# Optimization experiments

Hardware: AMD Instinct MI355X
Metric: run time of the kernel (lower is better)

## Reference

```python
import jax, jax.numpy as jnp
import numpy as np

N = 50000
E = 800000
F_IN = 128
HID = 64
HEADS = 4
NEG_SLOPE = 0.2  # PyG GATConv default negative_slope


def segment_softmax(e, dst, num_segments):
    # numerically stable softmax over edges grouped by destination node
    m = jax.ops.segment_max(e, dst, num_segments=num_segments)
    ex = jnp.exp(e - m[dst])
    s = jax.ops.segment_sum(ex, dst, num_segments=num_segments)
    return ex / (s[dst] + 1e-16)


def gat_conv(x, src, dst, W, a_src, a_dst, bias, heads, out_ch, concat):
    n = x.shape[0]
    h = (x @ W).reshape(n, heads, out_ch)          # [N,H,C]
    alpha_s = (h * a_src).sum(-1)                  # [N,H]
    alpha_d = (h * a_dst).sum(-1)                  # [N,H]
    e = jax.nn.leaky_relu(alpha_s[src] + alpha_d[dst], NEG_SLOPE)  # [E,H]
    alpha = segment_softmax(e, dst, n)             # [E,H]
    out = jax.ops.segment_sum(h[src] * alpha[:, :, None], dst, num_segments=n)  # [N,H,C]
    out = out.reshape(n, heads * out_ch) if concat else out.mean(axis=1)
    return out + bias


def setup_inputs() -> dict:
    key = jax.random.key(0)
    ks = jax.random.split(key, 16)

    def lin(k, i, o):
        return (jax.random.normal(k, (i, o), jnp.float32) / np.float32(np.sqrt(i)))

    def att(k, h, c):
        return jax.random.normal(k, (h, c), jnp.float32) * np.float32(0.1)

    x = jax.random.normal(ks[0], (N, F_IN), jnp.float32)
    edge_index = jax.random.randint(ks[1], (2, E), 0, N, dtype=jnp.int32)
    return {
        "x": x,
        "W_emb": lin(ks[2], F_IN, HID), "b_emb": jnp.zeros(HID, jnp.float32),
        "W0": lin(ks[3], HID, HEADS * HID), "as0": att(ks[4], HEADS, HID), "ad0": att(ks[5], HEADS, HID), "b0": jnp.zeros(HEADS * HID, jnp.float32),
        "W1": lin(ks[6], HEADS * HID, HEADS * HID), "as1": att(ks[7], HEADS, HID), "ad1": att(ks[8], HEADS, HID), "b1": jnp.zeros(HEADS * HID, jnp.float32),
        "W2": lin(ks[9], HEADS * HID, HID), "as2": att(ks[10], 1, HID), "ad2": att(ks[11], 1, HID), "b2": jnp.zeros(HID, jnp.float32),
        "Wo1": lin(ks[12], HID, HID // 2), "bo1": jnp.zeros(HID // 2, jnp.float32),
        "Wo2": lin(ks[13], HID // 2, 1), "bo2": jnp.zeros(1, jnp.float32),
        "edge_index": edge_index,
    }


def reference(x, W_emb, b_emb, W0, as0, ad0, b0, W1, as1, ad1, b1, W2, as2, ad2, b2, Wo1, bo1, Wo2, bo2, edge_index):
    n = x.shape[0]
    loop = jnp.arange(n, dtype=edge_index.dtype)  # PyG GATConv adds self-loops
    src = jnp.concatenate([edge_index[0], loop])
    dst = jnp.concatenate([edge_index[1], loop])
    h = jax.nn.relu(x @ W_emb + b_emb)
    h = jax.nn.relu(gat_conv(h, src, dst, W0, as0, ad0, b0, HEADS, HID, True))   # dropout=identity (eval)
    h = jax.nn.relu(gat_conv(h, src, dst, W1, as1, ad1, b1, HEADS, HID, True))
    h = gat_conv(h, src, dst, W2, as2, ad2, b2, 1, HID, False)
    h = jax.nn.relu(h @ Wo1 + bo1)
    return h @ Wo2 + bo2  # [N,1]
```

## Files before the change

### kernel.cpp

```cpp
#include <hip/hip_runtime.h>

typedef _Float16 h8_t __attribute__((ext_vector_type(8)));
typedef _Float16 h4_t __attribute__((ext_vector_type(4)));
typedef float floatx4 __attribute__((ext_vector_type(4)));

__device__ __forceinline__ float leaky(float v) { return v >= 0.f ? v : 0.2f * v; }

__global__ void hist_kernel(const int* __restrict__ dst, int E, int* __restrict__ cnt) {
    int e = blockIdx.x * blockDim.x + threadIdx.x;
    if (e < E) atomicAdd(&cnt[dst[e]], 1);
}

__global__ __launch_bounds__(256) void blocksum_kernel(const int* __restrict__ cnt, int N,
                                                       int* __restrict__ bsum) {
    __shared__ int red[256];
    int tid = threadIdx.x;
    int idx = blockIdx.x * 256 + tid;
    red[tid] = idx < N ? cnt[idx] + 1 : 0;
    __syncthreads();
#pragma unroll
    for (int off = 128; off >= 1; off >>= 1) {
        if (tid < off) red[tid] += red[tid + off];
        __syncthreads();
    }
    if (tid == 0) bsum[blockIdx.x] = red[0];
}

__global__ __launch_bounds__(256) void scanbsum_kernel(int* __restrict__ bsum, int nb,
                                                       int* __restrict__ total) {
    __shared__ int part[256];
    int tid = threadIdx.x;
    int per = (nb + 255) / 256;
    int s0 = tid * per, s1 = min(s0 + per, nb);
    int s = 0;
    for (int i = s0; i < s1; i++) s += bsum[i];
    part[tid] = s;
    __syncthreads();
    for (int off = 1; off < 256; off <<= 1) {
        int v = (tid >= off) ? part[tid - off] : 0;
        __syncthreads();
        part[tid] += v;
        __syncthreads();
    }
    int base = (tid == 0) ? 0 : part[tid - 1];
    for (int i = s0; i < s1; i++) {
        int v = bsum[i];
        bsum[i] = base;
        base += v;
    }
    if (tid == 255) *total = part[255];
}

__global__ __launch_bounds__(256) void rowptr_kernel(const int* __restrict__ cnt,
                                                     const int* __restrict__ bsum, int N,
                                                     int* __restrict__ row_ptr,
                                                     int* __restrict__ cursor) {
    __shared__ int lds[256];
    int tid = threadIdx.x;
    int idx = blockIdx.x * 256 + tid;
    int v = idx < N ? cnt[idx] + 1 : 0;
    lds[tid] = v;
    __syncthreads();
    for (int off = 1; off < 256; off <<= 1) {
        int t = (tid >= off) ? lds[tid - off] : 0;
        __syncthreads();
        lds[tid] += t;
        __syncthreads();
    }
    if (idx < N) {
        int p = bsum[blockIdx.x] + lds[tid] - v;
        row_ptr[idx] = p;
        cursor[idx] = p;
    }
}

__global__ void scatter_kernel(const int* __restrict__ src, const int* __restrict__ dst,
                               int E, int N, int* __restrict__ cursor, int* __restrict__ csr_src) {
    int e = blockIdx.x * blockDim.x + threadIdx.x;
    if (e >= E + N) return;
    int s, d;
    if (e < E) { s = src[e]; d = dst[e]; }
    else       { s = e - E;  d = s; }
    int pos = atomicAdd(&cursor[d], 1);
    csr_src[pos] = s;
}

__global__ void prep_weight_kernel(const float* __restrict__ W,
                                   _Float16* __restrict__ Wh, _Float16* __restrict__ Wl,
                                   int K, int N) {
    int idx = blockIdx.x * blockDim.x + threadIdx.x;
    if (idx >= K * N) return;
    int k = idx / N, n = idx % N;
    float v = W[idx];
    _Float16 hi = (_Float16)v;
    _Float16 lo = (_Float16)(v - (float)hi);
    size_t o = ((size_t)(k >> 3) * N + n) * 8 + (k & 7);
    Wh[o] = hi; Wl[o] = lo;
}

__global__ void prep_act_kernel(const float* __restrict__ X,
                                _Float16* __restrict__ Ph, _Float16* __restrict__ Pl,
                                int M, int Mpad, int Kg, int K) {
    int idx = blockIdx.x * blockDim.x + threadIdx.x;
    if (idx >= Mpad * Kg) return;
    int row = idx / Kg, kg = idx - row * Kg;
    float vs[8] = {0.f, 0.f, 0.f, 0.f, 0.f, 0.f, 0.f, 0.f};
    if (row < M) {
        const float4* p = (const float4*)(X + (size_t)row * K + kg * 8);
        float4 a = p[0], b = p[1];
        vs[0] = a.x; vs[1] = a.y; vs[2] = a.z; vs[3] = a.w;
        vs[4] = b.x; vs[5] = b.y; vs[6] = b.z; vs[7] = b.w;
    }
    h8_t hh, hl;
#pragma unroll
    for (int j = 0; j < 8; j++) {
        _Float16 hi = (_Float16)vs[j];
        hh[j] = hi;
        hl[j] = (_Float16)(vs[j] - (float)hi);
    }
    size_t o = ((size_t)kg * Mpad + row) * 8;
    *reinterpret_cast<h8_t*>(Ph + o) = hh;
    *reinterpret_cast<h8_t*>(Pl + o) = hl;
}

__global__ __launch_bounds__(256) void gemm_emb_kernel(
        const _Float16* __restrict__ Ah, const _Float16* __restrict__ Al,
        const _Float16* __restrict__ Bh, const _Float16* __restrict__ Bl,
        const float* __restrict__ bias,
        _Float16* __restrict__ Ph, _Float16* __restrict__ Pl,
        int Mpad, int M, int K) {
    const int Nn = 64;
    __shared__ _Float16 stH[4][16][72];
    __shared__ _Float16 stL[4][16][72];
    int tid = threadIdx.x;
    int wv = tid >> 6, lane = tid & 63;
    int m16 = lane & 15, quad = lane >> 4;
    int row0 = blockIdx.x * 128 + wv * 32;

    floatx4 acc[2][4];
#pragma unroll
    for (int t = 0; t < 2; t++)
#pragma unroll
        for (int c = 0; c < 4; c++)
#pragma unroll
            for (int i = 0; i < 4; i++) acc[t][c][i] = 0.f;

    size_t aoff = ((size_t)quad * Mpad + row0 + m16) * 8;
    size_t boff = ((size_t)quad * Nn + m16) * 8;
    const size_t aStep = (size_t)Mpad * 32;
    const size_t bStep = (size_t)Nn * 32;

    for (int kt = 0; kt < K; kt += 32) {
        h8_t ah0 = *reinterpret_cast<const h8_t*>(Ah + aoff);
        h8_t ah1 = *reinterpret_cast<const h8_t*>(Ah + aoff + 128);
        h8_t al0 = *reinterpret_cast<const h8_t*>(Al + aoff);
        h8_t al1 = *reinterpret_cast<const h8_t*>(Al + aoff + 128);
#pragma unroll
        for (int c = 0; c < 4; c++) {
            h8_t bh = *reinterpret_cast<const h8_t*>(Bh + boff + c * 128);
            h8_t bl = *reinterpret_cast<const h8_t*>(Bl + boff + c * 128);
            acc[0][c] = __builtin_amdgcn_mfma_f32_16x16x32_f16(ah0, bh, acc[0][c], 0, 0, 0);
            acc[1][c] = __builtin_amdgcn_mfma_f32_16x16x32_f16(ah1, bh, acc[1][c], 0, 0, 0);
            acc[0][c] = __builtin_amdgcn_mfma_f32_16x16x32_f16(ah0, bl, acc[0][c], 0, 0, 0);
            acc[1][c] = __builtin_amdgcn_mfma_f32_16x16x32_f16(ah1, bl, acc[1][c], 0, 0, 0);
            acc[0][c] = __builtin_amdgcn_mfma_f32_16x16x32_f16(al0, bh, acc[0][c], 0, 0, 0);
            acc[1][c] = __builtin_amdgcn_mfma_f32_16x16x32_f16(al1, bh, acc[1][c], 0, 0, 0);
        }
        aoff += aStep; boff += bStep;
    }

#pragma unroll
    for (int t = 0; t < 2; t++) {
#pragma unroll
        for (int c = 0; c < 4; c++) {
            float bv = bias[c * 16 + m16];
#pragma unroll
            for (int i = 0; i < 4; i++) {
                float v = fmaxf(acc[t][c][i] + bv, 0.f);
                _Float16 hi = (_Float16)v;
                stH[wv][quad * 4 + i][c * 16 + m16] = hi;
                stL[wv][quad * 4 + i][c * 16 + m16] = (_Float16)(v - (float)hi);
            }
        }
        __syncthreads();
        int rowChunk = row0 + t * 16;
#pragma unroll
        for (int it = 0; it < 2; it++) {
            int lid = it * 64 + lane;
            int kg = lid >> 4, rloc = lid & 15;
            h8_t vh = *reinterpret_cast<const h8_t*>(&stH[wv][rloc][kg * 8]);
            h8_t vl = *reinterpret_cast<const h8_t*>(&stL[wv][rloc][kg * 8]);
            size_t o = ((size_t)kg * Mpad + rowChunk + rloc) * 8;
            *reinterpret_cast<h8_t*>(Ph + o) = vh;
            *reinterpret_cast<h8_t*>(Pl + o) = vl;
        }
        __syncthreads();
    }
}

__global__ __launch_bounds__(256) void gemm_gat_kernel(
        const _Float16* __restrict__ Ah, const _Float16* __restrict__ Al,
        const _Float16* __restrict__ Bh, const _Float16* __restrict__ Bl,
        const float* __restrict__ a_src, const float* __restrict__ a_dst,
        _Float16* __restrict__ hOut, float* __restrict__ aS, float* __restrict__ aD,
        int Mpad, int M, int K) {
    const int Nn = 256;
    __shared__ _Float16 st[4][16][136];
    int tid = threadIdx.x;
    int wv = tid >> 6, lane = tid & 63;
    int m16 = lane & 15, quad = lane >> 4;
    int row0 = blockIdx.x * 128 + wv * 32;
    int colBase = blockIdx.y * 128;

    floatx4 acc[2][8];
#pragma unroll
    for (int t = 0; t < 2; t++)
#pragma unroll
        for (int c = 0; c < 8; c++)
#pragma unroll
            for (int i = 0; i < 4; i++) acc[t][c][i] = 0.f;

    size_t aoff = ((size_t)quad * Mpad + row0 + m16) * 8;
    size_t boff = ((size_t)quad * Nn + colBase + m16) * 8;
    const size_t aStep = (size_t)Mpad * 32;
    const size_t bStep = (size_t)Nn * 32;

    for (int kt = 0; kt < K; kt += 32) {
        h8_t ah0 = *reinterpret_cast<const h8_t*>(Ah + aoff);
        h8_t ah1 = *reinterpret_cast<const h8_t*>(Ah + aoff + 128);
        h8_t al0 = *reinterpret_cast<const h8_t*>(Al + aoff);
        h8_t al1 = *reinterpret_cast<const h8_t*>(Al + aoff + 128);
#pragma unroll
        for (int c = 0; c < 8; c++) {
            h8_t bh = *reinterpret_cast<const h8_t*>(Bh + boff + c * 128);
            h8_t bl = *reinterpret_cast<const h8_t*>(Bl + boff + c * 128);
            acc[0][c] = __builtin_amdgcn_mfma_f32_16x16x32_f16(ah0, bh, acc[0][c], 0, 0, 0);
            acc[1][c] = __builtin_amdgcn_mfma_f32_16x16x32_f16(ah1, bh, acc[1][c], 0, 0, 0);
            acc[0][c] = __builtin_amdgcn_mfma_f32_16x16x32_f16(ah0, bl, acc[0][c], 0, 0, 0);
            acc[1][c] = __builtin_amdgcn_mfma_f32_16x16x32_f16(ah1, bl, acc[1][c], 0, 0, 0);
            acc[0][c] = __builtin_amdgcn_mfma_f32_16x16x32_f16(al0, bh, acc[0][c], 0, 0, 0);
            acc[1][c] = __builtin_amdgcn_mfma_f32_16x16x32_f16(al1, bh, acc[1][c], 0, 0, 0);
        }
        aoff += aStep; boff += bStep;
    }

    float asv[8], adv[8];
#pragma unroll
    for (int c = 0; c < 8; c++) {
        asv[c] = a_src[colBase + c * 16 + m16];
        adv[c] = a_dst[colBase + c * 16 + m16];
    }
    int hb = colBase >> 6;
#pragma unroll
    for (int t = 0; t < 2; t++) {
#pragma unroll
        for (int i = 0; i < 4; i++) {
            int r = row0 + t * 16 + quad * 4 + i;
            float s0 = 0.f, d0 = 0.f, s1 = 0.f, d1 = 0.f;
#pragma unroll
            for (int c = 0; c < 8; c++) {
                float v = acc[t][c][i];
                if (c < 4) { s0 += v * asv[c]; d0 += v * adv[c]; }
                else       { s1 += v * asv[c]; d1 += v * adv[c]; }
            }
#pragma unroll
            for (int off = 1; off < 16; off <<= 1) {
                s0 += __shfl_xor(s0, off);
                d0 += __shfl_xor(d0, off);
                s1 += __shfl_xor(s1, off);
                d1 += __shfl_xor(d1, off);
            }
            if (m16 == 0 && r < M) {
                aS[r * 4 + hb] = s0;     aD[r * 4 + hb] = d0;
                aS[r * 4 + hb + 1] = s1; aD[r * 4 + hb + 1] = d1;
            }
        }
    }

#pragma unroll
    for (int t = 0; t < 2; t++) {
#pragma unroll
        for (int c = 0; c < 8; c++)
#pragma unroll
            for (int i = 0; i < 4; i++)
                st[wv][quad * 4 + i][c * 16 + m16] = (_Float16)acc[t][c][i];
        __syncthreads();
        int rowChunk = row0 + t * 16;
#pragma unroll
        for (int it = 0; it < 4; it++) {
            int lid = it * 64 + lane;
            int rloc = lid >> 4, u = lid & 15;
            h8_t v = *reinterpret_cast<const h8_t*>(&st[wv][rloc][u * 8]);
            *reinterpret_cast<h8_t*>(hOut + (size_t)(rowChunk + rloc) * 256 + colBase + u * 8) = v;
        }
        __syncthreads();
    }
}

__global__ __launch_bounds__(256) void gemm_l2_kernel(
        const _Float16* __restrict__ Ah, const _Float16* __restrict__ Al,
        const _Float16* __restrict__ Bh, const _Float16* __restrict__ Bl,
        const float* __restrict__ a_src, const float* __restrict__ a_dst,
        _Float16* __restrict__ hOut, float* __restrict__ aS, float* __restrict__ aD,
        int Mpad, int M, int K) {
    const int Nn = 64;
    __shared__ _Float16 st[4][16][72];
    int tid = threadIdx.x;
    int wv = tid >> 6, lane = tid & 63;
    int m16 = lane & 15, quad = lane >> 4;
    int row0 = blockIdx.x * 128 + wv * 32;

    floatx4 acc[2][4];
#pragma unroll
    for (int t = 0; t < 2; t++)
#pragma unroll
        for (int c = 0; c < 4; c++)
#pragma unroll
            for (int i = 0; i < 4; i++) acc[t][c][i] = 0.f;

    size_t aoff = ((size_t)quad * Mpad + row0 + m16) * 8;
    size_t boff = ((size_t)quad * Nn + m16) * 8;
    const size_t aStep = (size_t)Mpad * 32;
    const size_t bStep = (size_t)Nn * 32;

    for (int kt = 0; kt < K; kt += 32) {
        h8_t ah0 = *reinterpret_cast<const h8_t*>(Ah + aoff);
        h8_t ah1 = *reinterpret_cast<const h8_t*>(Ah + aoff + 128);
        h8_t al0 = *reinterpret_cast<const h8_t*>(Al + aoff);
        h8_t al1 = *reinterpret_cast<const h8_t*>(Al + aoff + 128);
#pragma unroll
        for (int c = 0; c < 4; c++) {
            h8_t bh = *reinterpret_cast<const h8_t*>(Bh + boff + c * 128);
            h8_t bl = *reinterpret_cast<const h8_t*>(Bl + boff + c * 128);
            acc[0][c] = __builtin_amdgcn_mfma_f32_16x16x32_f16(ah0, bh, acc[0][c], 0, 0, 0);
            acc[1][c] = __builtin_amdgcn_mfma_f32_16x16x32_f16(ah1, bh, acc[1][c], 0, 0, 0);
            acc[0][c] = __builtin_amdgcn_mfma_f32_16x16x32_f16(ah0, bl, acc[0][c], 0, 0, 0);
            acc[1][c] = __builtin_amdgcn_mfma_f32_16x16x32_f16(ah1, bl, acc[1][c], 0, 0, 0);
            acc[0][c] = __builtin_amdgcn_mfma_f32_16x16x32_f16(al0, bh, acc[0][c], 0, 0, 0);
            acc[1][c] = __builtin_amdgcn_mfma_f32_16x16x32_f16(al1, bh, acc[1][c], 0, 0, 0);
        }
        aoff += aStep; boff += bStep;
    }

    float asv[4], adv[4];
#pragma unroll
    for (int c = 0; c < 4; c++) {
        asv[c] = a_src[c * 16 + m16];
        adv[c] = a_dst[c * 16 + m16];
    }
#pragma unroll
    for (int t = 0; t < 2; t++) {
#pragma unroll
        for (int i = 0; i < 4; i++) {
            int r = row0 + t * 16 + quad * 4 + i;
            float s0 = 0.f, d0 = 0.f;
#pragma unroll
            for (int c = 0; c < 4; c++) {
                float v = acc[t][c][i];
                s0 += v * asv[c]; d0 += v * adv[c];
            }
#pragma unroll
            for (int off = 1; off < 16; off <<= 1) {
                s0 += __shfl_xor(s0, off);
                d0 += __shfl_xor(d0, off);
            }
            if (m16 == 0 && r < M) { aS[r] = s0; aD[r] = d0; }
        }
    }

#pragma unroll
    for (int t = 0; t < 2; t++) {
#pragma unroll
        for (int c = 0; c < 4; c++)
#pragma unroll
            for (int i = 0; i < 4; i++)
                st[wv][quad * 4 + i][c * 16 + m16] = (_Float16)acc[t][c][i];
        __syncthreads();
        int rowChunk = row0 + t * 16;
#pragma unroll
        for (int it = 0; it < 2; it++) {
            int lid = it * 64 + lane;
            int rloc = lid >> 3, u = lid & 7;
            h8_t v = *reinterpret_cast<const h8_t*>(&st[wv][rloc][u * 8]);
            *reinterpret_cast<h8_t*>(hOut + (size_t)(rowChunk + rloc) * 64 + u * 8) = v;
        }
        __syncthreads();
    }
}

__global__ __launch_bounds__(256) void aggregate4_kernel(const _Float16* __restrict__ hsrc,
                                                         const float* __restrict__ alpha_s,
                                                         const float* __restrict__ alpha_d,
                                                         const int* __restrict__ row_ptr,
                                                         const int* __restrict__ csr_src,
                                                         const float* __restrict__ bias,
                                                         _Float16* __restrict__ outH,
                                                         _Float16* __restrict__ outL,
                                                         int N, int Mpad) {
    __shared__ float wlds[4][64][4];
    __shared__ int   slds[4][64];
    int wv = threadIdx.x >> 6, lane = threadIdx.x & 63;
    int node = blockIdx.x * 4 + wv;
    if (node >= N) return;
    int rs = row_ptr[node], re = row_ptr[node + 1];
    int head = lane >> 4, c4 = (lane & 15) * 4;
    float4 ad4 = *(const float4*)(alpha_d + (size_t)node * 4);

    float m0 = -1e30f, m1 = -1e30f, m2 = -1e30f, m3 = -1e30f;
    for (int base = rs; base < re; base += 64) {
        int i = base + lane;
        if (i < re) {
            int s = csr_src[i];
            float4 as = *(const float4*)(alpha_s + (size_t)s * 4);
            m0 = fmaxf(m0, leaky(as.x + ad4.x));
            m1 = fmaxf(m1, leaky(as.y + ad4.y));
            m2 = fmaxf(m2, leaky(as.z + ad4.z));
            m3 = fmaxf(m3, leaky(as.w + ad4.w));
        }
    }
#pragma unroll
    for (int off = 32; off >= 1; off >>= 1) {
        m0 = fmaxf(m0, __shfl_xor(m0, off));
        m1 = fmaxf(m1, __shfl_xor(m1, off));
        m2 = fmaxf(m2, __shfl_xor(m2, off));
        m3 = fmaxf(m3, __shfl_xor(m3, off));
    }

    float den0 = 0.f, den1 = 0.f, den2 = 0.f, den3 = 0.f;
    float a0 = 0.f, a1 = 0.f, a2 = 0.f, a3 = 0.f;
    float* wp = &wlds[wv][0][0];
    int*   sp = &slds[wv][0];
    for (int base = rs; base < re; base += 64) {
        int i = base + lane;
        float w0 = 0.f, w1 = 0.f, w2 = 0.f, w3 = 0.f;
        int s = 0;
        if (i < re) {
            s = csr_src[i];
            float4 as = *(const float4*)(alpha_s + (size_t)s * 4);
            w0 = __expf(leaky(as.x + ad4.x) - m0);
            w1 = __expf(leaky(as.y + ad4.y) - m1);
            w2 = __expf(leaky(as.z + ad4.z) - m2);
            w3 = __expf(leaky(as.w + ad4.w) - m3);
        }
        den0 += w0; den1 += w1; den2 += w2; den3 += w3;
        sp[lane] = s;
        *(float4*)(wp + lane * 4) = make_float4(w0, w1, w2, w3);
        int cnt = min(64, re - base);
#pragma unroll 4
        for (int j = 0; j < cnt; j++) {
            int s2 = sp[j];
            float w = wp[j * 4 + head];
            h4_t hv = *reinterpret_cast<const h4_t*>(hsrc + (size_t)s2 * 256 + (head << 6) + c4);
            a0 += w * (float)hv[0]; a1 += w * (float)hv[1];
            a2 += w * (float)hv[2]; a3 += w * (float)hv[3];
        }
    }
#pragma unroll
    for (int off = 32; off >= 1; off >>= 1) {
        den0 += __shfl_xor(den0, off);
        den1 += __shfl_xor(den1, off);
        den2 += __shfl_xor(den2, off);
        den3 += __shfl_xor(den3, off);
    }
    float den = (head & 2) ? ((head & 1) ? den3 : den2) : ((head & 1) ? den1 : den0);
    float inv = 1.f / (den + 1e-16f);
    int cbase = (head << 6) + c4;
    float v0 = fmaxf(a0 * inv + bias[cbase + 0], 0.f);
    float v1 = fmaxf(a1 * inv + bias[cbase + 1], 0.f);
    float v2 = fmaxf(a2 * inv + bias[cbase + 2], 0.f);
    float v3 = fmaxf(a3 * inv + bias[cbase + 3], 0.f);
    h4_t hv, lv;
    _Float16 h;
    h = (_Float16)v0; hv[0] = h; lv[0] = (_Float16)(v0 - (float)h);
    h = (_Float16)v1; hv[1] = h; lv[1] = (_Float16)(v1 - (float)h);
    h = (_Float16)v2; hv[2] = h; lv[2] = (_Float16)(v2 - (float)h);
    h = (_Float16)v3; hv[3] = h; lv[3] = (_Float16)(v3 - (float)h);
    size_t o = ((size_t)(cbase >> 3) * Mpad + node) * 8 + (cbase & 7);
    *reinterpret_cast<h4_t*>(outH + o) = hv;
    *reinterpret_cast<h4_t*>(outL + o) = lv;
}

__global__ __launch_bounds__(256) void aggregate1_kernel(const _Float16* __restrict__ hsrc,
                                                         const float* __restrict__ alpha_s,
                                                         const float* __restrict__ alpha_d,
                                                         const int* __restrict__ row_ptr,
                                                         const int* __restrict__ csr_src,
                                                         const float* __restrict__ bias,
                                                         float* __restrict__ out, int N) {
    __shared__ float wlds[4][64];
    __shared__ int   slds[4][64];
    int wv = threadIdx.x >> 6, lane = threadIdx.x & 63;
    int node = blockIdx.x * 4 + wv;
    if (node >= N) return;
    int rs = row_ptr[node], re = row_ptr[node + 1];
    float ad = alpha_d[node];

    float m = -1e30f;
    for (int base = rs; base < re; base += 64) {
        int i = base + lane;
        if (i < re) {
            int s = csr_src[i];
            m = fmaxf(m, leaky(alpha_s[s] + ad));
        }
    }
#pragma unroll
    for (int off = 32; off >= 1; off >>= 1) m = fmaxf(m, __shfl_xor(m, off));

    float den = 0.f, acc = 0.f;
    float* wp = &wlds[wv][0];
    int*   sp = &slds[wv][0];
    for (int base = rs; base < re; base += 64) {
        int i = base + lane;
        float w = 0.f;
        int s = 0;
        if (i < re) {
            s = csr_src[i];
            w = __expf(leaky(alpha_s[s] + ad) - m);
        }
        den += w;
        sp[lane] = s;
        wp[lane] = w;
        int cnt = min(64, re - base);
#pragma unroll 4
        for (int j = 0; j < cnt; j++) {
            int s2 = sp[j];
            acc += wp[j] * (float)hsrc[(size_t)s2 * 64 + lane];
        }
    }
#pragma unroll
    for (int off = 32; off >= 1; off >>= 1) den += __shfl_xor(den, off);
    float v = acc / (den + 1e-16f) + bias[lane];
    out[(size_t)node * 64 + lane] = v;
}

__global__ __launch_bounds__(256) void mlp_head_kernel(const float* __restrict__ hin,
                                                       const float* __restrict__ Wo1,
                                                       const float* __restrict__ bo1,
                                                       const float* __restrict__ Wo2,
                                                       const float* __restrict__ bo2,
                                                       float* __restrict__ out, int N) {
    __shared__ float w1[64 * 32];
    __shared__ float w2[32];
    __shared__ float b1s[32];
    int tid = threadIdx.x;
#pragma unroll
    for (int i = 0; i < 8; i++) w1[tid + i * 256] = Wo1[tid + i * 256];
    if (tid < 32) { w2[tid] = Wo2[tid]; b1s[tid] = bo1[tid]; }
    __syncthreads();
    int n = blockIdx.x * blockDim.x + tid;
    if (n >= N) return;
    float hrow[64];
    const float* pr = hin + (size_t)n * 64;
#pragma unroll
    for (int i = 0; i < 64; i++) hrow[i] = pr[i];
    float sum = 0.f;
    for (int j = 0; j < 32; j++) {
        float a = b1s[j];
#pragma unroll
        for (int k = 0; k < 64; k++) a += hrow[k] * w1[k * 32 + j];
        a = fmaxf(a, 0.f);
        sum += a * w2[j];
    }
    out[n] = sum + bo2[0];
}

extern "C" void kernel_launch(void* const* d_in, const int* in_sizes, int n_in,
                              void* d_out, int out_size, void* d_ws, size_t ws_size,
                              hipStream_t stream) {
    const float* x     = (const float*)d_in[0];
    const float* W_emb = (const float*)d_in[1];
    const float* b_emb = (const float*)d_in[2];
    const float* W0    = (const float*)d_in[3];
    const float* as0   = (const float*)d_in[4];
    const float* ad0   = (const float*)d_in[5];
    const float* b0    = (const float*)d_in[6];
    const float* W1    = (const float*)d_in[7];
    const float* as1   = (const float*)d_in[8];
    const float* ad1   = (const float*)d_in[9];
    const float* b1    = (const float*)d_in[10];
    const float* W2    = (const float*)d_in[11];
    const float* as2   = (const float*)d_in[12];
    const float* ad2   = (const float*)d_in[13];
    const float* b2    = (const float*)d_in[14];
    const float* Wo1   = (const float*)d_in[15];
    const float* bo1   = (const float*)d_in[16];
    const float* Wo2   = (const float*)d_in[17];
    const float* bo2   = (const float*)d_in[18];
    const int* eidx    = (const int*)d_in[19];

    const int N = in_sizes[0] / 128;
    const int E = in_sizes[19] / 2;
    const int* esrc = eidx;
    const int* edst = eidx + E;
    const int gmB  = (N + 127) / 128;
    const int Mpad = gmB * 128;
    const int nb   = (N + 255) / 256;

    char* w = (char*)d_ws;
    auto alloc = [&](size_t bytes) {
        char* p = w;
        w += (bytes + 255) & ~(size_t)255;
        return (void*)p;
    };
    _Float16* hOut = (_Float16*)alloc((size_t)Mpad * 256 * 2);
    _Float16* PHh  = (_Float16*)alloc((size_t)Mpad * 256 * 2);
    _Float16* PHl  = (_Float16*)alloc((size_t)Mpad * 256 * 2);
    _Float16* XPh  = (_Float16*)alloc((size_t)Mpad * 128 * 2);
    _Float16* XPl  = (_Float16*)alloc((size_t)Mpad * 128 * 2);
    float* bufA    = (float*)alloc((size_t)Mpad * 64 * 4);
    float* aS      = (float*)alloc((size_t)N * 4 * 4);
    float* aD      = (float*)alloc((size_t)N * 4 * 4);
    int*   row_ptr = (int*)alloc((size_t)(N + 1) * 4);
    int*   cursor  = (int*)alloc((size_t)N * 4);
    int*   cnt     = (int*)alloc((size_t)N * 4);
    int*   bsum    = (int*)alloc((size_t)nb * 4);
    int*   csr     = (int*)alloc((size_t)(E + N) * 4);
    _Float16* WeH  = (_Float16*)alloc(128 * 64 * 2);
    _Float16* WeL  = (_Float16*)alloc(128 * 64 * 2);
    _Float16* W0H  = (_Float16*)alloc(64 * 256 * 2);
    _Float16* W0L  = (_Float16*)alloc(64 * 256 * 2);
    _Float16* W1H  = (_Float16*)alloc(256 * 256 * 2);
    _Float16* W1L  = (_Float16*)alloc(256 * 256 * 2);
    _Float16* W2H  = (_Float16*)alloc(256 * 64 * 2);
    _Float16* W2L  = (_Float16*)alloc(256 * 64 * 2);

    hipMemsetAsync(cnt, 0, (size_t)N * 4, stream);
    hist_kernel<<<(E + 255) / 256, 256, 0, stream>>>(edst, E, cnt);
    blocksum_kernel<<<nb, 256, 0, stream>>>(cnt, N, bsum);
    scanbsum_kernel<<<1, 256, 0, stream>>>(bsum, nb, row_ptr + N);
    rowptr_kernel<<<nb, 256, 0, stream>>>(cnt, bsum, N, row_ptr, cursor);
    scatter_kernel<<<(E + N + 255) / 256, 256, 0, stream>>>(esrc, edst, E, N, cursor, csr);

    prep_weight_kernel<<<(128 * 64 + 255) / 256, 256, 0, stream>>>(W_emb, WeH, WeL, 128, 64);
    prep_weight_kernel<<<(64 * 256 + 255) / 256, 256, 0, stream>>>(W0, W0H, W0L, 64, 256);
    prep_weight_kernel<<<(256 * 256 + 255) / 256, 256, 0, stream>>>(W1, W1H, W1L, 256, 256);
    prep_weight_kernel<<<(256 * 64 + 255) / 256, 256, 0, stream>>>(W2, W2H, W2L, 256, 64);

    int gn4 = (N + 3) / 4;

    prep_act_kernel<<<((size_t)Mpad * 16 + 255) / 256, 256, 0, stream>>>(x, XPh, XPl, N, Mpad, 16, 128);
    gemm_emb_kernel<<<dim3(gmB, 1), 256, 0, stream>>>(XPh, XPl, WeH, WeL, b_emb, PHh, PHl, Mpad, N, 128);

    gemm_gat_kernel<<<dim3(gmB, 2), 256, 0, stream>>>(PHh, PHl, W0H, W0L, as0, ad0, hOut, aS, aD, Mpad, N, 64);
    aggregate4_kernel<<<gn4, 256, 0, stream>>>(hOut, aS, aD, row_ptr, csr, b0, PHh, PHl, N, Mpad);

    gemm_gat_kernel<<<dim3(gmB, 2), 256, 0, stream>>>(PHh, PHl, W1H, W1L, as1, ad1, hOut, aS, aD, Mpad, N, 256);
    aggregate4_kernel<<<gn4, 256, 0, stream>>>(hOut, aS, aD, row_ptr, csr, b1, PHh, PHl, N, Mpad);

    gemm_l2_kernel<<<dim3(gmB, 1), 256, 0, stream>>>(PHh, PHl, W2H, W2L, as2, ad2, hOut, aS, aD, Mpad, N, 256);
    aggregate1_kernel<<<gn4, 256, 0, stream>>>(hOut, aS, aD, row_ptr, csr, b2, bufA, N);

    mlp_head_kernel<<<(N + 255) / 256, 256, 0, stream>>>(bufA, Wo1, bo1, Wo2, bo2, (float*)d_out, N);
}
```

Before: 528.9 us.

## Cache first-chunk logits, pack offsets with weights, vectorize single-head aggregation

Merges the four weight-prep launches into one 2D-grid kernel. In the 4-head aggregation, the first 64-edge chunk's source indices and leaky logits are cached in LDS so the softmax pass does not reload them, and byte offsets are packed with weights as int2 to simplify the gather's address arithmetic. The single-head aggregation now has each lane gather four fp16 channels from one of four interleaved edges and reduce across lane groups with shuffles, giving wider loads and fewer serial iterations. Template tags keep per-layer kernel instantiations apart. This adds LDS use, which may lower occupancy.

```diff
diff --git a/kernel.cpp b/kernel.cpp
--- a/kernel.cpp
+++ b/kernel.cpp
@@ -85,9 +85,20 @@
     csr_src[pos] = s;
 }
 
-__global__ void prep_weight_kernel(const float* __restrict__ W,
-                                   _Float16* __restrict__ Wh, _Float16* __restrict__ Wl,
-                                   int K, int N) {
+__global__ void prep_weights_all(const float* __restrict__ W_emb, const float* __restrict__ W0,
+                                 const float* __restrict__ W1, const float* __restrict__ W2,
+                                 _Float16* __restrict__ WeH, _Float16* __restrict__ WeL,
+                                 _Float16* __restrict__ W0H, _Float16* __restrict__ W0L,
+                                 _Float16* __restrict__ W1H, _Float16* __restrict__ W1L,
+                                 _Float16* __restrict__ W2H, _Float16* __restrict__ W2L) {
+    int which = blockIdx.y;
+    const float* W;
+    _Float16 *Wh, *Wl;
+    int K, N;
+    if (which == 0)      { W = W_emb; Wh = WeH; Wl = WeL; K = 128; N = 64; }
+    else if (which == 1) { W = W0;    Wh = W0H; Wl = W0L; K = 64;  N = 256; }
+    else if (which == 2) { W = W1;    Wh = W1H; Wl = W1L; K = 256; N = 256; }
+    else                 { W = W2;    Wh = W2H; Wl = W2L; K = 256; N = 64; }
     int idx = blockIdx.x * blockDim.x + threadIdx.x;
     if (idx >= K * N) return;
     int k = idx / N, n = idx % N;
@@ -198,6 +209,7 @@
     }
 }
 
+template <int TAG>
 __global__ __launch_bounds__(256) void gemm_gat_kernel(
         const _Float16* __restrict__ Ah, const _Float16* __restrict__ Al,
         const _Float16* __restrict__ Bh, const _Float16* __restrict__ Bl,
@@ -388,6 +400,7 @@
     }
 }
 
+template <int TAG>
 __global__ __launch_bounds__(256) void aggregate4_kernel(const _Float16* __restrict__ hsrc,
                                                          const float* __restrict__ alpha_s,
                                                          const float* __restrict__ alpha_d,
@@ -397,8 +410,9 @@
                                                          _Float16* __restrict__ outH,
                                                          _Float16* __restrict__ outL,
                                                          int N, int Mpad) {
-    __shared__ float wlds[4][64][4];
-    __shared__ int   slds[4][64];
+    __shared__ float4 lkc[4][64];
+    __shared__ int    scc[4][64];
+    __shared__ int2   pk[4][256];
     int wv = threadIdx.x >> 6, lane = threadIdx.x & 63;
     int node = blockIdx.x * 4 + wv;
     if (node >= N) return;
@@ -412,10 +426,11 @@
         if (i < re) {
             int s = csr_src[i];
             float4 as = *(const float4*)(alpha_s + (size_t)s * 4);
-            m0 = fmaxf(m0, leaky(as.x + ad4.x));
-            m1 = fmaxf(m1, leaky(as.y + ad4.y));
-            m2 = fmaxf(m2, leaky(as.z + ad4.z));
-            m3 = fmaxf(m3, leaky(as.w + ad4.w));
+            float4 lk = make_float4(leaky(as.x + ad4.x), leaky(as.y + ad4.y),
+                                    leaky(as.z + ad4.z), leaky(as.w + ad4.w));
+            if (base == rs) { lkc[wv][lane] = lk; scc[wv][lane] = s; }
+            m0 = fmaxf(m0, lk.x); m1 = fmaxf(m1, lk.y);
+            m2 = fmaxf(m2, lk.z); m3 = fmaxf(m3, lk.w);
         }
     }
 #pragma unroll
@@ -428,29 +443,37 @@
 
     float den0 = 0.f, den1 = 0.f, den2 = 0.f, den3 = 0.f;
     float a0 = 0.f, a1 = 0.f, a2 = 0.f, a3 = 0.f;
-    float* wp = &wlds[wv][0][0];
-    int*   sp = &slds[wv][0];
+    const char* hbase = (const char*)hsrc;
+    int cbyte = c4 * 2;
     for (int base = rs; base < re; base += 64) {
         int i = base + lane;
         float w0 = 0.f, w1 = 0.f, w2 = 0.f, w3 = 0.f;
-        int s = 0;
+        int off = 0;
         if (i < re) {
-            s = csr_src[i];
-            float4 as = *(const float4*)(alpha_s + (size_t)s * 4);
-            w0 = __expf(leaky(as.x + ad4.x) - m0);
-            w1 = __expf(leaky(as.y + ad4.y) - m1);
-            w2 = __expf(leaky(as.z + ad4.z) - m2);
-            w3 = __expf(leaky(as.w + ad4.w) - m3);
+            float4 lk;
+            int s;
+            if (base == rs) { lk = lkc[wv][lane]; s = scc[wv][lane]; }
+            else {
+                s = csr_src[i];
+                float4 as = *(const float4*)(alpha_s + (size_t)s * 4);
+                lk = make_float4(leaky(as.x + ad4.x), leaky(as.y + ad4.y),
+                                 leaky(as.z + ad4.z), leaky(as.w + ad4.w));
+            }
+            w0 = __expf(lk.x - m0); w1 = __expf(lk.y - m1);
+            w2 = __expf(lk.z - m2); w3 = __expf(lk.w - m3);
+            off = s * 512;
         }
         den0 += w0; den1 += w1; den2 += w2; den3 += w3;
-        sp[lane] = s;
-        *(float4*)(wp + lane * 4) = make_float4(w0, w1, w2, w3);
+        pk[wv][lane * 4 + 0] = make_int2(off,       __float_as_int(w0));
+        pk[wv][lane * 4 + 1] = make_int2(off + 128, __float_as_int(w1));
+        pk[wv][lane * 4 + 2] = make_int2(off + 256, __float_as_int(w2));
+        pk[wv][lane * 4 + 3] = make_int2(off + 384, __float_as_int(w3));
         int cnt = min(64, re - base);
 #pragma unroll 4
         for (int j = 0; j < cnt; j++) {
-            int s2 = sp[j];
-            float w = wp[j * 4 + head];
-            h4_t hv = *reinterpret_cast<const h4_t*>(hsrc + (size_t)s2 * 256 + (head << 6) + c4);
+            int2 t = pk[wv][j * 4 + head];
+            float w = __int_as_float(t.y);
+            h4_t hv = *reinterpret_cast<const h4_t*>(hbase + t.x + cbyte);
             a0 += w * (float)hv[0]; a1 += w * (float)hv[1];
             a2 += w * (float)hv[2]; a3 += w * (float)hv[3];
         }
@@ -487,13 +510,14 @@
                                                          const int* __restrict__ csr_src,
                                                          const float* __restrict__ bias,
                                                          float* __restrict__ out, int N) {
-    __shared__ float wlds[4][64];
-    __shared__ int   slds[4][64];
+    __shared__ int2 pk[4][64];
     int wv = threadIdx.x >> 6, lane = threadIdx.x & 63;
     int node = blockIdx.x * 4 + wv;
     if (node >= N) return;
     int rs = row_ptr[node], re = row_ptr[node + 1];
     float ad = alpha_d[node];
+    int e4 = lane >> 4, c4 = (lane & 15) * 4;
+    int cbyte = c4 * 2;
 
     float m = -1e30f;
     for (int base = rs; base < re; base += 64) {
@@ -506,31 +530,45 @@
 #pragma unroll
     for (int off = 32; off >= 1; off >>= 1) m = fmaxf(m, __shfl_xor(m, off));
 
-    float den = 0.f, acc = 0.f;
-    float* wp = &wlds[wv][0];
-    int*   sp = &slds[wv][0];
+    float den = 0.f;
+    float ax = 0.f, ay = 0.f, az = 0.f, aw = 0.f;
+    const char* hbase = (const char*)hsrc;
     for (int base = rs; base < re; base += 64) {
         int i = base + lane;
         float w = 0.f;
-        int s = 0;
+        int off = 0;
         if (i < re) {
-            s = csr_src[i];
+            int s = csr_src[i];
             w = __expf(leaky(alpha_s[s] + ad) - m);
+            off = s * 128;
         }
         den += w;
-        sp[lane] = s;
-        wp[lane] = w;
+        pk[wv][lane] = make_int2(off, __float_as_int(w));
         int cnt = min(64, re - base);
 #pragma unroll 4
-        for (int j = 0; j < cnt; j++) {
-            int s2 = sp[j];
-            acc += wp[j] * (float)hsrc[(size_t)s2 * 64 + lane];
-        }
-    }
+        for (int j = e4; j < cnt; j += 4) {
+            int2 t = pk[wv][j];
+            float wj = __int_as_float(t.y);
+            h4_t hv = *reinterpret_cast<const h4_t*>(hbase + t.x + cbyte);
+            ax += wj * (float)hv[0]; ay += wj * (float)hv[1];
+            az += wj * (float)hv[2]; aw += wj * (float)hv[3];
+        }
+    }
+    ax += __shfl_xor(ax, 16); ax += __shfl_xor(ax, 32);
+    ay += __shfl_xor(ay, 16); ay += __shfl_xor(ay, 32);
+    az += __shfl_xor(az, 16); az += __shfl_xor(az, 32);
+    aw += __shfl_xor(aw, 16); aw += __shfl_xor(aw, 32);
 #pragma unroll
     for (int off = 32; off >= 1; off >>= 1) den += __shfl_xor(den, off);
-    float v = acc / (den + 1e-16f) + bias[lane];
-    out[(size_t)node * 64 + lane] = v;
+    if (e4 == 0) {
+        float inv = 1.f / (den + 1e-16f);
+        float4 o;
+        o.x = ax * inv + bias[c4 + 0];
+        o.y = ay * inv + bias[c4 + 1];
+        o.z = az * inv + bias[c4 + 2];
+        o.w = aw * inv + bias[c4 + 3];
+        *(float4*)(out + (size_t)node * 64 + c4) = o;
+    }
 }
 
 __global__ __launch_bounds__(256) void mlp_head_kernel(const float* __restrict__ hin,
@@ -631,21 +669,19 @@
     rowptr_kernel<<<nb, 256, 0, stream>>>(cnt, bsum, N, row_ptr, cursor);
     scatter_kernel<<<(E + N + 255) / 256, 256, 0, stream>>>(esrc, edst, E, N, cursor, csr);
 
-    prep_weight_kernel<<<(128 * 64 + 255) / 256, 256, 0, stream>>>(W_emb, WeH, WeL, 128, 64);
-    prep_weight_kernel<<<(64 * 256 + 255) / 256, 256, 0, stream>>>(W0, W0H, W0L, 64, 256);
-    prep_weight_kernel<<<(256 * 256 + 255) / 256, 256, 0, stream>>>(W1, W1H, W1L, 256, 256);
-    prep_weight_kernel<<<(256 * 64 + 255) / 256, 256, 0, stream>>>(W2, W2H, W2L, 256, 64);
+    prep_weights_all<<<dim3(256, 4), 256, 0, stream>>>(W_emb, W0, W1, W2,
+                                                       WeH, WeL, W0H, W0L, W1H, W1L, W2H, W2L);
 
     int gn4 = (N + 3) / 4;
 
     prep_act_kernel<<<((size_t)Mpad * 16 + 255) / 256, 256, 0, stream>>>(x, XPh, XPl, N, Mpad, 16, 128);
     gemm_emb_kernel<<<dim3(gmB, 1), 256, 0, stream>>>(XPh, XPl, WeH, WeL, b_emb, PHh, PHl, Mpad, N, 128);
 
-    gemm_gat_kernel<<<dim3(gmB, 2), 256, 0, stream>>>(PHh, PHl, W0H, W0L, as0, ad0, hOut, aS, aD, Mpad, N, 64);
-    aggregate4_kernel<<<gn4, 256, 0, stream>>>(hOut, aS, aD, row_ptr, csr, b0, PHh, PHl, N, Mpad);
-
-    gemm_gat_kernel<<<dim3(gmB, 2), 256, 0, stream>>>(PHh, PHl, W1H, W1L, as1, ad1, hOut, aS, aD, Mpad, N, 256);
-    aggregate4_kernel<<<gn4, 256, 0, stream>>>(hOut, aS, aD, row_ptr, csr, b1, PHh, PHl, N, Mpad);
+    gemm_gat_kernel<0><<<dim3(gmB, 2), 256, 0, stream>>>(PHh, PHl, W0H, W0L, as0, ad0, hOut, aS, aD, Mpad, N, 64);
+    aggregate4_kernel<0><<<gn4, 256, 0, stream>>>(hOut, aS, aD, row_ptr, csr, b0, PHh, PHl, N, Mpad);
+
+    gemm_gat_kernel<1><<<dim3(gmB, 2), 256, 0, stream>>>(PHh, PHl, W1H, W1L, as1, ad1, hOut, aS, aD, Mpad, N, 256);
+    aggregate4_kernel<1><<<gn4, 256, 0, stream>>>(hOut, aS, aD, row_ptr, csr, b1, PHh, PHl, N, Mpad);
 
     gemm_l2_kernel<<<dim3(gmB, 1), 256, 0, stream>>>(PHh, PHl, W2H, W2L, as2, ad2, hOut, aS, aD, Mpad, N, 256);
     aggregate1_kernel<<<gn4, 256, 0, stream>>>(hOut, aS, aD, row_ptr, csr, b2, bufA, N);
```

New measurement: 515.1 us. 1.03x faster.
